# Performance work log

Hardware: AMD Instinct MI355X
Metric: run time of the kernel (lower is better)

The kernel has to match this reference:

```python
import jax, jax.numpy as jnp
import numpy as np

TOTAL = 131072          # total sentences
DIM = 690               # relation_dim (PCNN: 3*230)
NUM_CLASSES = 53        # NYT-10 relations
TOTAL_TYPE = 324        # type_num^2 = 18^2
NUM_BAGS = 8192
ALPHA = 0.9


def setup_inputs() -> dict:
    key = jax.random.key(0)
    ks = jax.random.split(key, 8)
    x = jax.random.normal(ks[0], (TOTAL, DIM), dtype=jnp.float32)
    # strictly increasing bag boundaries: scope[0]=0, scope[-1]=TOTAL, all bags non-empty
    rng = np.random.default_rng(0)
    cuts = np.sort(rng.choice(np.arange(1, TOTAL), NUM_BAGS - 1, replace=False))
    input_scope = jnp.asarray(np.concatenate([[0], cuts, [TOTAL]]), dtype=jnp.int32)
    type_label = jax.random.randint(ks[1], (TOTAL,), 0, TOTAL_TYPE, dtype=jnp.int32)
    query = jax.random.randint(ks[2], (TOTAL,), 0, NUM_CLASSES, dtype=jnp.int32)
    # learned parameters (xavier-ish scale)
    rel_scale = (6.0 / (NUM_CLASSES + DIM)) ** 0.5
    typ_scale = (6.0 / (TOTAL_TYPE + DIM)) ** 0.5
    lin_scale = (6.0 / (DIM + TOTAL_TYPE)) ** 0.5
    relation_weight = jax.random.uniform(ks[3], (NUM_CLASSES, DIM), jnp.float32, -rel_scale, rel_scale)
    type_weight = jax.random.uniform(ks[4], (TOTAL_TYPE, DIM), jnp.float32, -typ_scale, typ_scale)
    bias = jax.random.normal(ks[5], (NUM_CLASSES,), dtype=jnp.float32)
    liner_w = jax.random.uniform(ks[6], (TOTAL_TYPE, DIM), jnp.float32, -lin_scale, lin_scale)
    liner_b = jnp.zeros((TOTAL_TYPE,), dtype=jnp.float32)
    return {
        "x": x, "input_scope": input_scope, "type_label": type_label, "query": query,
        "relation_weight": relation_weight, "type_weight": type_weight, "bias": bias,
        "liner_w": liner_w, "liner_b": liner_b,
    }


def reference(x, input_scope, type_label, query, relation_weight, type_weight, bias, liner_w, liner_b):
    # ---- soft_type (beta != 0 branch) ----
    type_logits = jax.nn.softmax(x @ liner_w.T + liner_b, axis=1)          # [total, T2]
    max_scores = jnp.max(type_logits, axis=1, keepdims=True)               # [total, 1]
    one_hot = jax.nn.one_hot(type_label, TOTAL_TYPE, dtype=type_logits.dtype)
    nscore = type_logits + ALPHA * max_scores * one_hot
    soft_label = jnp.argmax(nscore, axis=1)                                # [total]

    # ---- _train_logits: per-sentence attention logits ----
    xt = x + type_weight[soft_label]                                       # [total, D]
    att = jnp.sum(xt * relation_weight[query], axis=1)                     # [total]

    # ---- bag-wise segment softmax + weighted sum over scopes ----
    seg = jnp.searchsorted(input_scope, jnp.arange(TOTAL), side="right") - 1  # [total] bag ids
    m = jax.ops.segment_max(att, seg, num_segments=NUM_BAGS)               # [bags]
    p = jnp.exp(att - m[seg])
    s = jax.ops.segment_sum(p, seg, num_segments=NUM_BAGS)                 # [bags]
    score = p / s[seg]                                                     # [total]
    bag_repre = jax.ops.segment_sum(score[:, None] * x, seg, num_segments=NUM_BAGS)  # [bags, D]

    # ---- _logits ----
    logits = bag_repre @ relation_weight.T + bias                          # [bags, C]
    return logits, type_logits
```

## Files before the change

### kernel.cpp

```cpp
#include <hip/hip_runtime.h>
#include <hip/hip_bf16.h>

#define TOTAL   131072
#define DIMK    690
#define KPAD    704
#define KSTEPS  22
#define NCLASS  53
#define NTYPE   324
#define NCOLS   377
#define NPAD    384
#define NBAGS   8192
#define ALPHA   0.9f
#define TAU     1e-5f
#define FLAGCAP 32768
#define ZS      388

typedef short  bf16x4 __attribute__((ext_vector_type(4)));
typedef short  bf16x8 __attribute__((ext_vector_type(8)));
typedef float  f32x4  __attribute__((ext_vector_type(4)));

__device__ __forceinline__ unsigned short bf16_rne(float f) {
    unsigned int u = __float_as_uint(f);
    u = (u + 0x7fffu + ((u >> 16) & 1u)) >> 16;
    return (unsigned short)u;
}
__device__ __forceinline__ float bf16f(unsigned short h) {
    return __uint_as_float(((unsigned int)h) << 16);
}

__global__ __launch_bounds__(256) void k_pack(const float* __restrict__ liner_w,
                                              const float* __restrict__ rel_w,
                                              unsigned short* __restrict__ whP,
                                              unsigned short* __restrict__ wlP) {
    const int id = blockIdx.x * 256 + threadIdx.x;
    if (id >= NPAD * KPAD) return;
    const int n = id / KPAD, k = id % KPAD;
    float v = 0.f;
    if (k < DIMK) {
        if (n < NTYPE)      v = liner_w[(size_t)n * DIMK + k];
        else if (n < NCOLS) v = rel_w[(size_t)(n - NTYPE) * DIMK + k];
    }
    const unsigned short hi = bf16_rne(v);
    const unsigned short lo = bf16_rne(v - bf16f(hi));
    const int t = n >> 4, col = n & 15, s = k >> 5, kk = k & 31;
    const int lane = (kk >> 3) * 16 + col, j = kk & 7;
    const int pidx = ((t * KSTEPS + s) * 64 + lane) * 8 + j;
    whP[pidx] = hi;
    wlP[pidx] = lo;
}

__global__ __launch_bounds__(256) void k_table(const float* __restrict__ tw,
                                               const float* __restrict__ rw,
                                               float* __restrict__ table) {
    const int pair = blockIdx.x * 4 + (threadIdx.x >> 6);
    const int lane = threadIdx.x & 63;
    if (pair >= NTYPE * NCLASS) return;
    const int s = pair / NCLASS;
    const int q = pair % NCLASS;
    const float* a = tw + (size_t)s * DIMK;
    const float* b = rw + (size_t)q * DIMK;
    float acc = 0.f;
    for (int k = lane; k < DIMK; k += 64) acc += a[k] * b[k];
#pragma unroll
    for (int off = 32; off; off >>= 1) acc += __shfl_xor(acc, off);
    if (lane == 0) table[pair] = acc;
}

template<int H>
__device__ __forceinline__ void epi8(f32x4 (&acc)[4][3],
                                     float* __restrict__ zS,
                                     const float* __restrict__ sB,
                                     const int* __restrict__ type_label,
                                     const int* __restrict__ query,
                                     const float* __restrict__ table,
                                     float* __restrict__ type_logits,
                                     float* __restrict__ att,
                                     float* __restrict__ xr,
                                     int* __restrict__ flagcnt,
                                     int* __restrict__ flaglist,
                                     int base, int wv, int ln) {
    constexpr int MT = H >> 1;
    constexpr int Q0 = (H & 1) * 2;
    const int q = ln >> 4;

    if (q == Q0 || q == Q0 + 1) {
        const int lr0 = (q - Q0) * 4;
#pragma unroll
        for (int nt = 0; nt < 3; ++nt) {
            const int col = wv * 48 + nt * 16 + (ln & 15);
            const float bb = sB[col];
#pragma unroll
            for (int rg = 0; rg < 4; ++rg)
                zS[(lr0 + rg) * ZS + col] = acc[MT][nt][rg] + bb;
        }
    }
    asm volatile("s_waitcnt lgkmcnt(0)" ::: "memory");
    __builtin_amdgcn_s_barrier();

    const int grow = base + H * 8 + wv;
    const float* zrow = &zS[wv * ZS];

    float z[6];
#pragma unroll
    for (int j = 0; j < 6; ++j) {
        const int c = ln + 64 * j;
        z[j] = (c < NTYPE) ? zrow[c] : -INFINITY;
    }
    float m = -INFINITY;
#pragma unroll
    for (int j = 0; j < 6; ++j) m = fmaxf(m, z[j]);
#pragma unroll
    for (int off = 32; off; off >>= 1) m = fmaxf(m, __shfl_xor(m, off));

    float e[6];
    float ssum = 0.f;
#pragma unroll
    for (int j = 0; j < 6; ++j) {
        const int c = ln + 64 * j;
        e[j] = 0.f;
        if (c < NTYPE) { e[j] = __expf(z[j] - m); ssum += e[j]; }
    }
#pragma unroll
    for (int off = 32; off; off >>= 1) ssum += __shfl_xor(ssum, off);
    const float inv = 1.0f / ssum;

    const int label = type_label[grow];
    float bestv = -INFINITY;
    int   besti = NTYPE;
#pragma unroll
    for (int j = 0; j < 6; ++j) {
        const int c = ln + 64 * j;
        if (c < NTYPE) {
            const float p = e[j] * inv;
            type_logits[(size_t)grow * NTYPE + c] = p;
            const float v = p + ((c == label) ? ALPHA * inv : 0.f);
            if (v > bestv || (v == bestv && c < besti)) { bestv = v; besti = c; }
        }
    }
#pragma unroll
    for (int off = 32; off; off >>= 1) {
        const float ov = __shfl_xor(bestv, off);
        const int   oi = __shfl_xor(besti, off);
        if (ov > bestv || (ov == bestv && oi < besti)) { bestv = ov; besti = oi; }
    }

    float sv = -INFINITY;
#pragma unroll
    for (int j = 0; j < 6; ++j) {
        const int c = ln + 64 * j;
        if (c < NTYPE && c != besti) {
            const float v = e[j] * inv + ((c == label) ? ALPHA * inv : 0.f);
            sv = fmaxf(sv, v);
        }
    }
#pragma unroll
    for (int off = 32; off; off >>= 1) sv = fmaxf(sv, __shfl_xor(sv, off));

    if (ln == 0) {
        const int qq = query[grow];
        att[grow] = zrow[NTYPE + qq] + table[besti * NCLASS + qq];
        if (bestv - sv < TAU) {
            const int ix = atomicAdd(flagcnt, 1);
            if (ix < FLAGCAP) flaglist[ix] = grow;
        }
    }
    if (ln < NCLASS)
        xr[(size_t)grow * NCLASS + ln] = zrow[NTYPE + ln];

    asm volatile("s_waitcnt lgkmcnt(0)" ::: "memory");
    __builtin_amdgcn_s_barrier();
}

__global__ __launch_bounds__(512, 4) void k_main(const float* __restrict__ x,
                                                 const int* __restrict__ type_label,
                                                 const int* __restrict__ query,
                                                 const unsigned short* __restrict__ whP,
                                                 const unsigned short* __restrict__ wlP,
                                                 const float* __restrict__ liner_b,
                                                 const float* __restrict__ table,
                                                 float* __restrict__ type_logits,
                                                 float* __restrict__ att,
                                                 float* __restrict__ xr,
                                                 int* __restrict__ flagcnt,
                                                 int* __restrict__ flaglist) {
    __shared__ unsigned short aS[2][2][2048];
    __shared__ float sB[NPAD];

    const int tid  = threadIdx.x;
    const int base = blockIdx.x * 64;
    const int wv   = tid >> 6;
    const int ln   = tid & 63;

    const int srow  = tid >> 3;
    const int kpart = tid & 7;

    f32x4 acc[4][3];
#pragma unroll
    for (int mt = 0; mt < 4; ++mt)
#pragma unroll
        for (int nt = 0; nt < 3; ++nt)
            acc[mt][nt] = (f32x4){0.f, 0.f, 0.f, 0.f};

    auto load_x = [&](int s, float (&dst)[4]) {
        const int k0 = s * 32 + kpart * 4;
        const float* xp = x + (size_t)(base + srow) * DIMK + k0;
        if (k0 + 4 <= DIMK) {
            const float2 p0 = *(const float2*)(xp + 0);
            const float2 p1 = *(const float2*)(xp + 2);
            dst[0] = p0.x; dst[1] = p0.y; dst[2] = p1.x; dst[3] = p1.y;
        } else {
#pragma unroll
            for (int j = 0; j < 4; ++j) dst[j] = (k0 + j < DIMK) ? xp[j] : 0.f;
        }
    };
    auto write_a = [&](int nb, const float (&src)[4]) {
        const int kb = kpart >> 1, j0 = (kpart & 1) * 4;
        const int widx = (kb * 64 + srow) * 8 + j0;
        bf16x4 hv, lv;
#pragma unroll
        for (int j = 0; j < 4; ++j) {
            const unsigned short h = bf16_rne(src[j]);
            hv[j] = (short)h;
            lv[j] = (short)bf16_rne(src[j] - bf16f(h));
        }
        *(bf16x4*)&aS[nb][0][widx] = hv;
        *(bf16x4*)&aS[nb][1][widx] = lv;
    };

    float xv[4];
    load_x(0, xv);
    write_a(0, xv);
    for (int c = tid; c < NPAD; c += 512) sB[c] = (c < NTYPE) ? liner_b[c] : 0.f;
    asm volatile("s_waitcnt lgkmcnt(0)" ::: "memory");
    __builtin_amdgcn_s_barrier();

    const int aidx_base = ((ln >> 4) * 64 + (ln & 15)) * 8;
    for (int s = 0; s < KSTEPS; ++s) {
        const int cur = s & 1;
        float xn[4];
        if (s + 1 < KSTEPS) load_x(s + 1, xn);

        bf16x8 ah[4], al[4];
#pragma unroll
        for (int mt = 0; mt < 4; ++mt) {
            const int aidx = aidx_base + mt * 128;
            ah[mt] = *(const bf16x8*)&aS[cur][0][aidx];
            al[mt] = *(const bf16x8*)&aS[cur][1][aidx];
        }
#pragma unroll
        for (int nt = 0; nt < 3; ++nt) {
            const int ntg = wv * 3 + nt;
            const size_t boff = ((size_t)(ntg * KSTEPS + s) * 64 + ln) * 8;
            const bf16x8 bh = *(const bf16x8*)(whP + boff);
            const bf16x8 bl = *(const bf16x8*)(wlP + boff);
#pragma unroll
            for (int mt = 0; mt < 4; ++mt) {
                acc[mt][nt] = __builtin_amdgcn_mfma_f32_16x16x32_bf16(ah[mt], bh, acc[mt][nt], 0, 0, 0);
                acc[mt][nt] = __builtin_amdgcn_mfma_f32_16x16x32_bf16(ah[mt], bl, acc[mt][nt], 0, 0, 0);
                acc[mt][nt] = __builtin_amdgcn_mfma_f32_16x16x32_bf16(al[mt], bh, acc[mt][nt], 0, 0, 0);
            }
        }
        if (s + 1 < KSTEPS) write_a(1 - cur, xn);
        asm volatile("s_waitcnt lgkmcnt(0)" ::: "memory");
        __builtin_amdgcn_s_barrier();
    }

    float* zS = (float*)aS;
    epi8<0>(acc, zS, sB, type_label, query, table, type_logits, att, xr, flagcnt, flaglist, base, wv, ln);
    epi8<1>(acc, zS, sB, type_label, query, table, type_logits, att, xr, flagcnt, flaglist, base, wv, ln);
    epi8<2>(acc, zS, sB, type_label, query, table, type_logits, att, xr, flagcnt, flaglist, base, wv, ln);
    epi8<3>(acc, zS, sB, type_label, query, table, type_logits, att, xr, flagcnt, flaglist, base, wv, ln);
    epi8<4>(acc, zS, sB, type_label, query, table, type_logits, att, xr, flagcnt, flaglist, base, wv, ln);
    epi8<5>(acc, zS, sB, type_label, query, table, type_logits, att, xr, flagcnt, flaglist, base, wv, ln);
    epi8<6>(acc, zS, sB, type_label, query, table, type_logits, att, xr, flagcnt, flaglist, base, wv, ln);
    epi8<7>(acc, zS, sB, type_label, query, table, type_logits, att, xr, flagcnt, flaglist, base, wv, ln);
}

__global__ __launch_bounds__(256) void k_fix(const float* __restrict__ x,
                                             const float* __restrict__ liner_w,
                                             const float* __restrict__ liner_b,
                                             const int* __restrict__ type_label,
                                             const int* __restrict__ query,
                                             const float* __restrict__ table,
                                             const float* __restrict__ xr,
                                             const int* __restrict__ flagcnt,
                                             const int* __restrict__ flaglist,
                                             float* __restrict__ att) {
    __shared__ float xs[704];
    __shared__ float zs[NTYPE];
    __shared__ float redm[4];
    __shared__ float redv[4];
    __shared__ int   redi[4];
    const int tid = threadIdx.x;
    const int wv  = tid >> 6;
    const int ln  = tid & 63;
    int count = *flagcnt;
    if (count > FLAGCAP) count = FLAGCAP;

    for (int f = blockIdx.x; f < count; f += gridDim.x) {
        const int row = flaglist[f];
        __syncthreads();
        for (int k = tid; k < 704; k += 256) xs[k] = (k < DIMK) ? x[(size_t)row * DIMK + k] : 0.f;
        __syncthreads();

        for (int ci = 0; ci < 81; ++ci) {
            const int c = wv * 81 + ci;
            const float* w = liner_w + (size_t)c * DIMK;
            float acc = 0.f;
#pragma unroll
            for (int kk = 0; kk < 11; ++kk) {
                const int k = ln + kk * 64;
                const float wval = (k < DIMK) ? w[k] : 0.f;
                acc = fmaf(xs[k], wval, acc);
            }
#pragma unroll
            for (int off = 32; off; off >>= 1) acc += __shfl_xor(acc, off);
            if (ln == 0) zs[c] = acc + liner_b[c];
        }
        __syncthreads();

        float z0 = (tid < NTYPE) ? zs[tid] : -INFINITY;
        const int c1 = tid + 256;
        float z1 = (c1 < NTYPE) ? zs[c1] : -INFINITY;
        float m = fmaxf(z0, z1);
#pragma unroll
        for (int off = 32; off; off >>= 1) m = fmaxf(m, __shfl_xor(m, off));
        if (ln == 0) redm[wv] = m;
        __syncthreads();
        m = fmaxf(fmaxf(redm[0], redm[1]), fmaxf(redm[2], redm[3]));

        const int label = type_label[row];
        const float u0 = (tid < NTYPE) ? (__expf(z0 - m) + ((tid == label) ? ALPHA : 0.f)) : -1.f;
        const float u1 = (c1 < NTYPE)  ? (__expf(z1 - m) + ((c1 == label) ? ALPHA : 0.f))  : -1.f;
        float bv = u0; int bi = tid;
        if (u1 > bv) { bv = u1; bi = c1; }
#pragma unroll
        for (int off = 32; off; off >>= 1) {
            const float ov = __shfl_xor(bv, off);
            const int   oi = __shfl_xor(bi, off);
            if (ov > bv || (ov == bv && oi < bi)) { bv = ov; bi = oi; }
        }
        if (ln == 0) { redv[wv] = bv; redi[wv] = bi; }
        __syncthreads();
        if (tid == 0) {
            float fbv = redv[0]; int fbi = redi[0];
#pragma unroll
            for (int w = 1; w < 4; ++w) {
                if (redv[w] > fbv || (redv[w] == fbv && redi[w] < fbi)) {
                    fbv = redv[w]; fbi = redi[w];
                }
            }
            const int q = query[row];
            att[row] = xr[(size_t)row * NCLASS + q] + table[fbi * NCLASS + q];
        }
    }
}

__global__ __launch_bounds__(64) void k_bag(const float* __restrict__ att,
                                            const float* __restrict__ xr,
                                            const int* __restrict__ scope,
                                            const float* __restrict__ bias,
                                            float* __restrict__ logits) {
    const int b = blockIdx.x;
    const int lane = threadIdx.x;
    const int s0 = scope[b];
    const int s1 = scope[b + 1];

    float m = -INFINITY;
    for (int i = s0 + lane; i < s1; i += 64) m = fmaxf(m, att[i]);
#pragma unroll
    for (int off = 32; off; off >>= 1) m = fmaxf(m, __shfl_xor(m, off));

    float sum = 0.f;
    float acc = 0.f;
    for (int i0 = s0; i0 < s1; i0 += 64) {
        const int n = min(64, s1 - i0);
        float e = 0.f;
        if (lane < n) e = __expf(att[i0 + lane] - m);
        float es = e;
#pragma unroll
        for (int off = 32; off; off >>= 1) es += __shfl_xor(es, off);
        sum += es;
        for (int j = 0; j < n; ++j) {
            const float ej = __shfl(e, j);
            if (lane < NCLASS) acc = fmaf(ej, xr[(size_t)(i0 + j) * NCLASS + lane], acc);
        }
    }
    const float inv = 1.0f / sum;
    if (lane < NCLASS) logits[b * NCLASS + lane] = acc * inv + bias[lane];
}

extern "C" void kernel_launch(void* const* d_in, const int* in_sizes, int n_in,
                              void* d_out, int out_size, void* d_ws, size_t ws_size,
                              hipStream_t stream) {
    const float* x          = (const float*)d_in[0];
    const int*   scope      = (const int*)d_in[1];
    const int*   type_label = (const int*)d_in[2];
    const int*   query      = (const int*)d_in[3];
    const float* rel_w      = (const float*)d_in[4];
    const float* type_w     = (const float*)d_in[5];
    const float* bias       = (const float*)d_in[6];
    const float* liner_w    = (const float*)d_in[7];
    const float* liner_b    = (const float*)d_in[8];

    float* logits      = (float*)d_out;
    float* type_logits = (float*)d_out + NBAGS * NCLASS;

    float* ws = (float*)d_ws;
    float*          table    = ws;
    float*          att      = ws + 17408;
    float*          xr       = ws + 148480;
    unsigned short* whP      = (unsigned short*)(ws + 7095296);
    unsigned short* wlP      = (unsigned short*)(ws + 7230464);
    int*            flagcnt  = (int*)(ws + 7365632);
    int*            flaglist = (int*)(ws + 7365633);

    hipMemsetAsync(flagcnt, 0, sizeof(int), stream);
    hipLaunchKernelGGL(k_pack, dim3((NPAD * KPAD + 255) / 256), dim3(256), 0, stream,
                       liner_w, rel_w, whP, wlP);
    hipLaunchKernelGGL(k_table, dim3((NTYPE * NCLASS + 3) / 4), dim3(256), 0, stream,
                       type_w, rel_w, table);
    hipLaunchKernelGGL(k_main, dim3(TOTAL / 64), dim3(512), 0, stream,
                       x, type_label, query, whP, wlP, liner_b, table,
                       type_logits, att, xr, flagcnt, flaglist);
    hipLaunchKernelGGL(k_fix, dim3(1024), dim3(256), 0, stream,
                       x, liner_w, liner_b, type_label, query, table, xr,
                       flagcnt, flaglist, att);
    hipLaunchKernelGGL(k_bag, dim3(NBAGS), dim3(64), 0, stream,
                       att, xr, scope, bias, logits);
}
```

Measured before the change: 438.4 us.

## Prefetch next-step B fragments, use packed bf16 convert, relax launch bounds

The main GEMM loop now prefetches the high-part weight fragments for the next K step into registers, with the loop unrolled by two to ping-pong the buffers. Global-load latency for B can then overlap the MFMAs of the current step. The fp32-to-bf16 hi/lo split of x now uses the hardware v_cvt_pk_bf16_f32 instruction instead of manual rounding. Launch bounds drop from 4 to 2 blocks per CU, giving more registers for the prefetch buffers at the cost of possible occupancy.

```diff
diff --git a/kernel.cpp b/kernel.cpp
--- a/kernel.cpp
+++ b/kernel.cpp
@@ -15,7 +15,6 @@
 #define FLAGCAP 32768
 #define ZS      388
 
-typedef short  bf16x4 __attribute__((ext_vector_type(4)));
 typedef short  bf16x8 __attribute__((ext_vector_type(8)));
 typedef float  f32x4  __attribute__((ext_vector_type(4)));
 
@@ -26,6 +25,11 @@
 }
 __device__ __forceinline__ float bf16f(unsigned short h) {
     return __uint_as_float(((unsigned int)h) << 16);
+}
+__device__ __forceinline__ unsigned cvtpk(float a, float b) {
+    unsigned r;
+    asm("v_cvt_pk_bf16_f32 %0, %1, %2" : "=v"(r) : "v"(a), "v"(b));
+    return r;
 }
 
 __global__ __launch_bounds__(256) void k_pack(const float* __restrict__ liner_w,
@@ -171,7 +175,7 @@
     __builtin_amdgcn_s_barrier();
 }
 
-__global__ __launch_bounds__(512, 4) void k_main(const float* __restrict__ x,
+__global__ __launch_bounds__(512, 2) void k_main(const float* __restrict__ x,
                                                  const int* __restrict__ type_label,
                                                  const int* __restrict__ query,
                                                  const unsigned short* __restrict__ whP,
@@ -201,6 +205,15 @@
         for (int nt = 0; nt < 3; ++nt)
             acc[mt][nt] = (f32x4){0.f, 0.f, 0.f, 0.f};
 
+    const unsigned short* whB[3];
+    const unsigned short* wlB[3];
+#pragma unroll
+    for (int nt = 0; nt < 3; ++nt) {
+        const int ntg = wv * 3 + nt;
+        whB[nt] = whP + ((size_t)(ntg * KSTEPS) * 64 + ln) * 8;
+        wlB[nt] = wlP + ((size_t)(ntg * KSTEPS) * 64 + ln) * 8;
+    }
+
     auto load_x = [&](int s, float (&dst)[4]) {
         const int k0 = s * 32 + kpart * 4;
         const float* xp = x + (size_t)(base + srow) * DIMK + k0;
@@ -216,29 +229,44 @@
     auto write_a = [&](int nb, const float (&src)[4]) {
         const int kb = kpart >> 1, j0 = (kpart & 1) * 4;
         const int widx = (kb * 64 + srow) * 8 + j0;
-        bf16x4 hv, lv;
-#pragma unroll
-        for (int j = 0; j < 4; ++j) {
-            const unsigned short h = bf16_rne(src[j]);
-            hv[j] = (short)h;
-            lv[j] = (short)bf16_rne(src[j] - bf16f(h));
-        }
-        *(bf16x4*)&aS[nb][0][widx] = hv;
-        *(bf16x4*)&aS[nb][1][widx] = lv;
+        const unsigned h01 = cvtpk(src[0], src[1]);
+        const unsigned h23 = cvtpk(src[2], src[3]);
+        const float r0 = src[0] - __uint_as_float(h01 << 16);
+        const float r1 = src[1] - __uint_as_float(h01 & 0xffff0000u);
+        const float r2 = src[2] - __uint_as_float(h23 << 16);
+        const float r3 = src[3] - __uint_as_float(h23 & 0xffff0000u);
+        const unsigned l01 = cvtpk(r0, r1);
+        const unsigned l23 = cvtpk(r2, r3);
+        *(uint2*)&aS[nb][0][widx] = make_uint2(h01, h23);
+        *(uint2*)&aS[nb][1][widx] = make_uint2(l01, l23);
     };
 
     float xv[4];
     load_x(0, xv);
     write_a(0, xv);
+    bf16x8 bhA[3], bhB[3];
+#pragma unroll
+    for (int nt = 0; nt < 3; ++nt) bhA[nt] = *(const bf16x8*)(whB[nt]);
     for (int c = tid; c < NPAD; c += 512) sB[c] = (c < NTYPE) ? liner_b[c] : 0.f;
     asm volatile("s_waitcnt lgkmcnt(0)" ::: "memory");
     __builtin_amdgcn_s_barrier();
 
     const int aidx_base = ((ln >> 4) * 64 + (ln & 15)) * 8;
-    for (int s = 0; s < KSTEPS; ++s) {
-        const int cur = s & 1;
+
+    auto kstep = [&](int s, int cur, bf16x8 (&bhC)[3], bf16x8 (&bhN)[3]) {
         float xn[4];
         if (s + 1 < KSTEPS) load_x(s + 1, xn);
+
+        const int so = s * 512;
+        bf16x8 bl[3];
+#pragma unroll
+        for (int nt = 0; nt < 3; ++nt)
+            bl[nt] = *(const bf16x8*)(wlB[nt] + so);
+        if (s + 1 < KSTEPS) {
+#pragma unroll
+            for (int nt = 0; nt < 3; ++nt)
+                bhN[nt] = *(const bf16x8*)(whB[nt] + so + 512);
+        }
 
         bf16x8 ah[4], al[4];
 #pragma unroll
@@ -249,20 +277,21 @@
         }
 #pragma unroll
         for (int nt = 0; nt < 3; ++nt) {
-            const int ntg = wv * 3 + nt;
-            const size_t boff = ((size_t)(ntg * KSTEPS + s) * 64 + ln) * 8;
-            const bf16x8 bh = *(const bf16x8*)(whP + boff);
-            const bf16x8 bl = *(const bf16x8*)(wlP + boff);
 #pragma unroll
             for (int mt = 0; mt < 4; ++mt) {
-                acc[mt][nt] = __builtin_amdgcn_mfma_f32_16x16x32_bf16(ah[mt], bh, acc[mt][nt], 0, 0, 0);
-                acc[mt][nt] = __builtin_amdgcn_mfma_f32_16x16x32_bf16(ah[mt], bl, acc[mt][nt], 0, 0, 0);
-                acc[mt][nt] = __builtin_amdgcn_mfma_f32_16x16x32_bf16(al[mt], bh, acc[mt][nt], 0, 0, 0);
+                acc[mt][nt] = __builtin_amdgcn_mfma_f32_16x16x32_bf16(ah[mt], bhC[nt], acc[mt][nt], 0, 0, 0);
+                acc[mt][nt] = __builtin_amdgcn_mfma_f32_16x16x32_bf16(ah[mt], bl[nt],  acc[mt][nt], 0, 0, 0);
+                acc[mt][nt] = __builtin_amdgcn_mfma_f32_16x16x32_bf16(al[mt], bhC[nt], acc[mt][nt], 0, 0, 0);
             }
         }
         if (s + 1 < KSTEPS) write_a(1 - cur, xn);
         asm volatile("s_waitcnt lgkmcnt(0)" ::: "memory");
         __builtin_amdgcn_s_barrier();
+    };
+
+    for (int s2 = 0; s2 < KSTEPS; s2 += 2) {
+        kstep(s2,     0, bhA, bhB);
+        kstep(s2 + 1, 1, bhB, bhA);
     }
 
     float* zS = (float*)aS;
```

Result: slower. 574.3 us (+31.0%).

## Stage 32 rows per epilogue pass and use packed bf16 conversion

Applied to the files above, without the earlier changes.

The epilogue now writes two M-tiles (32 rows) into a larger shared staging buffer per pass instead of 8 rows, so the 64-row block needs 2 passes and 4 barriers rather than 8 passes and 16. Each wave then handles 4 rows in a loop. The hi/lo bf16 split of x now uses the v_cvt_pk_bf16_f32 instruction instead of manual rounding. Shared memory grows to about 50KB (32*388 floats) through a union with the A buffers, which may reduce occupancy below the 4 blocks per CU that the launch bounds request.

```diff
diff --git a/kernel.cpp b/kernel.cpp
--- a/kernel.cpp
+++ b/kernel.cpp
@@ -15,7 +15,6 @@
 #define FLAGCAP 32768
 #define ZS      388
 
-typedef short  bf16x4 __attribute__((ext_vector_type(4)));
 typedef short  bf16x8 __attribute__((ext_vector_type(8)));
 typedef float  f32x4  __attribute__((ext_vector_type(4)));
 
@@ -26,6 +25,11 @@
 }
 __device__ __forceinline__ float bf16f(unsigned short h) {
     return __uint_as_float(((unsigned int)h) << 16);
+}
+__device__ __forceinline__ unsigned cvtpk(float a, float b) {
+    unsigned r;
+    asm("v_cvt_pk_bf16_f32 %0, %1, %2" : "=v"(r) : "v"(a), "v"(b));
+    return r;
 }
 
 __global__ __launch_bounds__(256) void k_pack(const float* __restrict__ liner_w,
@@ -66,106 +70,111 @@
     if (lane == 0) table[pair] = acc;
 }
 
-template<int H>
-__device__ __forceinline__ void epi8(f32x4 (&acc)[4][3],
-                                     float* __restrict__ zS,
-                                     const float* __restrict__ sB,
-                                     const int* __restrict__ type_label,
-                                     const int* __restrict__ query,
-                                     const float* __restrict__ table,
-                                     float* __restrict__ type_logits,
-                                     float* __restrict__ att,
-                                     float* __restrict__ xr,
-                                     int* __restrict__ flagcnt,
-                                     int* __restrict__ flaglist,
-                                     int base, int wv, int ln) {
-    constexpr int MT = H >> 1;
-    constexpr int Q0 = (H & 1) * 2;
+union EpiU {
+    unsigned short aS[2][2][2048];
+    float          zS[32 * ZS];
+};
+
+template<int SC>
+__device__ __forceinline__ void epi32(f32x4 (&acc)[4][3],
+                                      float* __restrict__ zS,
+                                      const float* __restrict__ sB,
+                                      const int* __restrict__ type_label,
+                                      const int* __restrict__ query,
+                                      const float* __restrict__ table,
+                                      float* __restrict__ type_logits,
+                                      float* __restrict__ att,
+                                      float* __restrict__ xr,
+                                      int* __restrict__ flagcnt,
+                                      int* __restrict__ flaglist,
+                                      int base, int wv, int ln) {
     const int q = ln >> 4;
 
-    if (q == Q0 || q == Q0 + 1) {
-        const int lr0 = (q - Q0) * 4;
-#pragma unroll
-        for (int nt = 0; nt < 3; ++nt) {
-            const int col = wv * 48 + nt * 16 + (ln & 15);
-            const float bb = sB[col];
-#pragma unroll
-            for (int rg = 0; rg < 4; ++rg)
-                zS[(lr0 + rg) * ZS + col] = acc[MT][nt][rg] + bb;
+#pragma unroll
+    for (int nt = 0; nt < 3; ++nt) {
+        const int col = wv * 48 + nt * 16 + (ln & 15);
+        const float bb = sB[col];
+#pragma unroll
+        for (int rg = 0; rg < 4; ++rg) {
+            zS[(q * 4 + rg) * ZS + col]      = acc[2 * SC + 0][nt][rg] + bb;
+            zS[(16 + q * 4 + rg) * ZS + col] = acc[2 * SC + 1][nt][rg] + bb;
         }
     }
     asm volatile("s_waitcnt lgkmcnt(0)" ::: "memory");
     __builtin_amdgcn_s_barrier();
 
-    const int grow = base + H * 8 + wv;
-    const float* zrow = &zS[wv * ZS];
-
-    float z[6];
-#pragma unroll
-    for (int j = 0; j < 6; ++j) {
-        const int c = ln + 64 * j;
-        z[j] = (c < NTYPE) ? zrow[c] : -INFINITY;
-    }
-    float m = -INFINITY;
-#pragma unroll
-    for (int j = 0; j < 6; ++j) m = fmaxf(m, z[j]);
-#pragma unroll
-    for (int off = 32; off; off >>= 1) m = fmaxf(m, __shfl_xor(m, off));
-
-    float e[6];
-    float ssum = 0.f;
-#pragma unroll
-    for (int j = 0; j < 6; ++j) {
-        const int c = ln + 64 * j;
-        e[j] = 0.f;
-        if (c < NTYPE) { e[j] = __expf(z[j] - m); ssum += e[j]; }
-    }
-#pragma unroll
-    for (int off = 32; off; off >>= 1) ssum += __shfl_xor(ssum, off);
-    const float inv = 1.0f / ssum;
-
-    const int label = type_label[grow];
-    float bestv = -INFINITY;
-    int   besti = NTYPE;
-#pragma unroll
-    for (int j = 0; j < 6; ++j) {
-        const int c = ln + 64 * j;
-        if (c < NTYPE) {
-            const float p = e[j] * inv;
-            type_logits[(size_t)grow * NTYPE + c] = p;
-            const float v = p + ((c == label) ? ALPHA * inv : 0.f);
-            if (v > bestv || (v == bestv && c < besti)) { bestv = v; besti = c; }
-        }
-    }
-#pragma unroll
-    for (int off = 32; off; off >>= 1) {
-        const float ov = __shfl_xor(bestv, off);
-        const int   oi = __shfl_xor(besti, off);
-        if (ov > bestv || (ov == bestv && oi < besti)) { bestv = ov; besti = oi; }
-    }
-
-    float sv = -INFINITY;
-#pragma unroll
-    for (int j = 0; j < 6; ++j) {
-        const int c = ln + 64 * j;
-        if (c < NTYPE && c != besti) {
-            const float v = e[j] * inv + ((c == label) ? ALPHA * inv : 0.f);
-            sv = fmaxf(sv, v);
-        }
-    }
-#pragma unroll
-    for (int off = 32; off; off >>= 1) sv = fmaxf(sv, __shfl_xor(sv, off));
-
-    if (ln == 0) {
-        const int qq = query[grow];
-        att[grow] = zrow[NTYPE + qq] + table[besti * NCLASS + qq];
-        if (bestv - sv < TAU) {
-            const int ix = atomicAdd(flagcnt, 1);
-            if (ix < FLAGCAP) flaglist[ix] = grow;
-        }
-    }
-    if (ln < NCLASS)
-        xr[(size_t)grow * NCLASS + ln] = zrow[NTYPE + ln];
+    for (int rr = 0; rr < 4; ++rr) {
+        const int lr   = wv * 4 + rr;
+        const int grow = base + SC * 32 + lr;
+        const float* zrow = &zS[lr * ZS];
+
+        float z[6];
+#pragma unroll
+        for (int j = 0; j < 6; ++j) {
+            const int c = ln + 64 * j;
+            z[j] = (c < NTYPE) ? zrow[c] : -INFINITY;
+        }
+        float m = -INFINITY;
+#pragma unroll
+        for (int j = 0; j < 6; ++j) m = fmaxf(m, z[j]);
+#pragma unroll
+        for (int off = 32; off; off >>= 1) m = fmaxf(m, __shfl_xor(m, off));
+
+        float e[6];
+        float ssum = 0.f;
+#pragma unroll
+        for (int j = 0; j < 6; ++j) {
+            const int c = ln + 64 * j;
+            e[j] = 0.f;
+            if (c < NTYPE) { e[j] = __expf(z[j] - m); ssum += e[j]; }
+        }
+#pragma unroll
+        for (int off = 32; off; off >>= 1) ssum += __shfl_xor(ssum, off);
+        const float inv = 1.0f / ssum;
+
+        const int label = type_label[grow];
+        float bestv = -INFINITY;
+        int   besti = NTYPE;
+#pragma unroll
+        for (int j = 0; j < 6; ++j) {
+            const int c = ln + 64 * j;
+            if (c < NTYPE) {
+                const float p = e[j] * inv;
+                type_logits[(size_t)grow * NTYPE + c] = p;
+                const float v = p + ((c == label) ? ALPHA * inv : 0.f);
+                if (v > bestv || (v == bestv && c < besti)) { bestv = v; besti = c; }
+            }
+        }
+#pragma unroll
+        for (int off = 32; off; off >>= 1) {
+            const float ov = __shfl_xor(bestv, off);
+            const int   oi = __shfl_xor(besti, off);
+            if (ov > bestv || (ov == bestv && oi < besti)) { bestv = ov; besti = oi; }
+        }
+
+        float sv = -INFINITY;
+#pragma unroll
+        for (int j = 0; j < 6; ++j) {
+            const int c = ln + 64 * j;
+            if (c < NTYPE && c != besti) {
+                const float v = e[j] * inv + ((c == label) ? ALPHA * inv : 0.f);
+                sv = fmaxf(sv, v);
+            }
+        }
+#pragma unroll
+        for (int off = 32; off; off >>= 1) sv = fmaxf(sv, __shfl_xor(sv, off));
+
+        if (ln == 0) {
+            const int qq = query[grow];
+            att[grow] = zrow[NTYPE + qq] + table[besti * NCLASS + qq];
+            if (bestv - sv < TAU) {
+                const int ix = atomicAdd(flagcnt, 1);
+                if (ix < FLAGCAP) flaglist[ix] = grow;
+            }
+        }
+        if (ln < NCLASS)
+            xr[(size_t)grow * NCLASS + ln] = zrow[NTYPE + ln];
+    }
 
     asm volatile("s_waitcnt lgkmcnt(0)" ::: "memory");
     __builtin_amdgcn_s_barrier();
@@ -183,7 +192,7 @@
                                                  float* __restrict__ xr,
                                                  int* __restrict__ flagcnt,
                                                  int* __restrict__ flaglist) {
-    __shared__ unsigned short aS[2][2][2048];
+    __shared__ __align__(16) EpiU uni;
     __shared__ float sB[NPAD];
 
     const int tid  = threadIdx.x;
@@ -216,15 +225,16 @@
     auto write_a = [&](int nb, const float (&src)[4]) {
         const int kb = kpart >> 1, j0 = (kpart & 1) * 4;
         const int widx = (kb * 64 + srow) * 8 + j0;
-        bf16x4 hv, lv;
-#pragma unroll
-        for (int j = 0; j < 4; ++j) {
-            const unsigned short h = bf16_rne(src[j]);
-            hv[j] = (short)h;
-            lv[j] = (short)bf16_rne(src[j] - bf16f(h));
-        }
-        *(bf16x4*)&aS[nb][0][widx] = hv;
-        *(bf16x4*)&aS[nb][1][widx] = lv;
+        const unsigned h01 = cvtpk(src[0], src[1]);
+        const unsigned h23 = cvtpk(src[2], src[3]);
+        const float r0 = src[0] - __uint_as_float(h01 << 16);
+        const float r1 = src[1] - __uint_as_float(h01 & 0xffff0000u);
+        const float r2 = src[2] - __uint_as_float(h23 << 16);
+        const float r3 = src[3] - __uint_as_float(h23 & 0xffff0000u);
+        const unsigned l01 = cvtpk(r0, r1);
+        const unsigned l23 = cvtpk(r2, r3);
+        *(uint2*)&uni.aS[nb][0][widx] = make_uint2(h01, h23);
+        *(uint2*)&uni.aS[nb][1][widx] = make_uint2(l01, l23);
     };
 
     float xv[4];
@@ -244,8 +254,8 @@
 #pragma unroll
         for (int mt = 0; mt < 4; ++mt) {
             const int aidx = aidx_base + mt * 128;
-            ah[mt] = *(const bf16x8*)&aS[cur][0][aidx];
-            al[mt] = *(const bf16x8*)&aS[cur][1][aidx];
+            ah[mt] = *(const bf16x8*)&uni.aS[cur][0][aidx];
+            al[mt] = *(const bf16x8*)&uni.aS[cur][1][aidx];
         }
 #pragma unroll
         for (int nt = 0; nt < 3; ++nt) {
@@ -265,15 +275,10 @@
         __builtin_amdgcn_s_barrier();
     }
 
-    float* zS = (float*)aS;
-    epi8<0>(acc, zS, sB, type_label, query, table, type_logits, att, xr, flagcnt, flaglist, base, wv, ln);
-    epi8<1>(acc, zS, sB, type_label, query, table, type_logits, att, xr, flagcnt, flaglist, base, wv, ln);
-    epi8<2>(acc, zS, sB, type_label, query, table, type_logits, att, xr, flagcnt, flaglist, base, wv, ln);
-    epi8<3>(acc, zS, sB, type_label, query, table, type_logits, att, xr, flagcnt, flaglist, base, wv, ln);
-    epi8<4>(acc, zS, sB, type_label, query, table, type_logits, att, xr, flagcnt, flaglist, base, wv, ln);
-    epi8<5>(acc, zS, sB, type_label, query, table, type_logits, att, xr, flagcnt, flaglist, base, wv, ln);
-    epi8<6>(acc, zS, sB, type_label, query, table, type_logits, att, xr, flagcnt, flaglist, base, wv, ln);
-    epi8<7>(acc, zS, sB, type_label, query, table, type_logits, att, xr, flagcnt, flaglist, base, wv, ln);
+    epi32<0>(acc, uni.zS, sB, type_label, query, table, type_logits, att, xr,
+             flagcnt, flaglist, base, wv, ln);
+    epi32<1>(acc, uni.zS, sB, type_label, query, table, type_logits, att, xr,
+             flagcnt, flaglist, base, wv, ln);
 }
 
 __global__ __launch_bounds__(256) void k_fix(const float* __restrict__ x,
```

Result: no change. 443.3 us (+1.1%).
